# Kernel optimization log

Measured on AMD Instinct MI355X. Metric: run time of the kernel, lower is better.

Reference implementation:

```python
import jax, jax.numpy as jnp
import numpy as np


def gcn_conv(x, src, dst, ew, W, b):
    """PyG GCNConv with edge weights: add self-loops, symmetric deg norm,
    x @ W then normalized scatter-add aggregation, plus bias."""
    N = x.shape[0]
    loop = jnp.arange(N)
    src2 = jnp.concatenate([src, loop])
    dst2 = jnp.concatenate([dst, loop])
    ew2 = jnp.concatenate([ew, jnp.ones((N,), dtype=x.dtype)])
    deg = jax.ops.segment_sum(ew2, dst2, num_segments=N)
    dis = jnp.where(deg > 0, jax.lax.rsqrt(jnp.maximum(deg, 1e-30)), 0.0)
    norm = dis[src2] * ew2 * dis[dst2]            # [E+N]
    h = x @ W                                      # [N, F]
    msg = h[src2] * norm[:, None]                  # gather + scale
    out = jax.ops.segment_sum(msg, dst2, num_segments=N)  # scatter-add
    return out + b


def setup_inputs() -> dict:
    key = jax.random.key(0)
    ks = jax.random.split(key, 12)
    N, F, E, H = 50000, 128, 625000, 121
    x = jax.random.normal(ks[0], (N, F), dtype=jnp.float32)
    edge_index = jax.random.randint(ks[1], (2, E), 0, N, dtype=jnp.int64)
    edge_attr = jax.random.uniform(ks[2], (E,), dtype=jnp.float32)
    s = 1.0 / np.sqrt(F)
    W1 = jax.random.uniform(ks[3], (F, F), minval=-s, maxval=s)
    b1 = jnp.zeros((F,), dtype=jnp.float32)
    W2 = jax.random.uniform(ks[4], (F, F), minval=-s, maxval=s)
    b2 = jnp.zeros((F,), dtype=jnp.float32)
    lw1 = jax.random.uniform(ks[5], (F, H), minval=-s, maxval=s)
    lb1 = jax.random.uniform(ks[6], (H,), minval=-s, maxval=s)
    sh = 1.0 / np.sqrt(H)
    lw2 = jax.random.uniform(ks[7], (H, 1), minval=-sh, maxval=sh)
    lb2 = jax.random.uniform(ks[8], (1,), minval=-sh, maxval=sh)
    return {"x": x, "edge_index": edge_index, "edge_attr": edge_attr,
            "W1": W1, "b1": b1, "W2": W2, "b2": b2,
            "lw1": lw1, "lb1": lb1, "lw2": lw2, "lb2": lb2}


def reference(x, edge_index, edge_attr, W1, b1, W2, b2, lw1, lb1, lw2, lb2):
    src, dst = edge_index[0], edge_index[1]
    h = jax.nn.relu(gcn_conv(x, src, dst, edge_attr, W1, b1))
    h = jax.nn.relu(gcn_conv(h, src, dst, edge_attr, W2, b2))
    g = jnp.mean(h, axis=0)                        # graph readout [F]
    g = jax.nn.relu(g @ lw1 + lb1)
    return g @ lw2 + lb2                           # [1]
```

## Files before the change

kernel.cpp:

```cpp
#include <hip/hip_runtime.h>
#include <hip/hip_bf16.h>

#define FDIM 128
#define ELLW 64
#define CHUNK 4096
#define BKTSH 8
#define CAP 4096

typedef unsigned int uint;
typedef unsigned short ushort;
typedef unsigned char uchar;
typedef __attribute__((ext_vector_type(8))) short bf16x8;
typedef __attribute__((ext_vector_type(4))) float f32x4;

__device__ __forceinline__ ushort f2bf(float f) {
    uint u = __float_as_uint(f);
    return (ushort)((u + 0x7fffu + ((u >> 16) & 1u)) >> 16);
}
__device__ __forceinline__ float bfhi(uint v) { return __uint_as_float(v & 0xffff0000u); }
__device__ __forceinline__ uchar f2fp8(float f) {
    return (uchar)(__builtin_amdgcn_cvt_pk_fp8_f32(f, 0.f, 0, false) & 0xff);
}

__global__ void prep(const float* __restrict__ W1, const float* __restrict__ W2,
                     ushort* __restrict__ wt1, ushort* __restrict__ wt2,
                     int* __restrict__ gcursor, float* __restrict__ partial2,
                     int nbkt) {
    int i = blockIdx.x * 256 + threadIdx.x;
    if (i < 16384) {
        int k = i >> 7, c = i & 127;
        wt1[c * FDIM + k] = f2bf(W1[i]);
    } else {
        int j = i - 16384;
        int k = j >> 7, c = j & 127;
        wt2[c * FDIM + k] = f2bf(W2[j]);
    }
    if (i < nbkt) gcursor[i] = i * CAP;
    if (i < 64 * FDIM) partial2[i] = 0.f;
}

__global__ __launch_bounds__(256)
void build_p1(const int* __restrict__ srcs, const int* __restrict__ dsts,
              const float* __restrict__ ew, int* gcursor,
              uint2* __restrict__ part, int E, int nbkt) {
    __shared__ int hist[256];
    __shared__ int gbase[256];
    __shared__ int cur[256];
    int tid = threadIdx.x;
    hist[tid] = 0;
    __syncthreads();
    int base = blockIdx.x * CHUNK;
    #pragma unroll
    for (int i = 0; i < CHUNK / 256; ++i) {
        int e = base + i * 256 + tid;
        if (e < E) atomicAdd(&hist[dsts[e] >> BKTSH], 1);
    }
    __syncthreads();
    if (tid < nbkt && hist[tid] > 0)
        gbase[tid] = atomicAdd(&gcursor[tid], hist[tid]);
    cur[tid] = 0;
    __syncthreads();
    #pragma unroll
    for (int i = 0; i < CHUNK / 256; ++i) {
        int e = base + i * 256 + tid;
        if (e < E) {
            int d = dsts[e];
            int bkt = d >> BKTSH;
            int pos = atomicAdd(&cur[bkt], 1);
            long gp = (long)gbase[bkt] + pos;
            if (gp < (long)(bkt + 1) * CAP)
                part[gp] = make_uint2(((uint)f2bf(ew[e]) << 16) | (uint)srcs[e],
                                      (uint)d);
        }
    }
}

__global__ __launch_bounds__(256)
void build_p2(const uint2* __restrict__ part, const int* __restrict__ gcursor,
              uint* __restrict__ ell, int* __restrict__ cnt,
              float* __restrict__ dis, int N) {
    __shared__ int lcur[256];
    __shared__ float ldeg[256];
    int tid = threadIdx.x;
    int b = blockIdx.x;
    lcur[tid] = 0; ldeg[tid] = 0.f;
    __syncthreads();
    int start = b * CAP;
    int end = min(gcursor[b], start + CAP);
    for (int e = start + tid; e < end; e += 256) {
        uint2 pe = part[e];
        int li = (int)pe.y - (b << BKTSH);
        int r = atomicAdd(&lcur[li], 1);
        if (r < ELLW) ell[(long)pe.y * ELLW + r] = pe.x;
        atomicAdd(&ldeg[li], bfhi(pe.x));
    }
    __syncthreads();
    int d = (b << BKTSH) + tid;
    if (d < N) {
        cnt[d] = min(lcur[tid], ELLW);
        dis[d] = rsqrtf(1.0f + ldeg[tid]);
    }
}

template<int IN_BF16>
__global__ __launch_bounds__(256) void gemm_mfma(const void* __restrict__ Ap,
                                                 const ushort* __restrict__ Wt,
                                                 const float* __restrict__ dis,
                                                 uchar* __restrict__ Hb, int N) {
    int lane = threadIdx.x & 63;
    int wave = threadIdx.x >> 6;
    int row0 = blockIdx.x * 64 + wave * 16;
    int m = lane & 15;
    int ko = (lane >> 4) << 3;
    int row = row0 + m;

    f32x4 acc[8];
    #pragma unroll
    for (int n = 0; n < 8; ++n) acc[n] = (f32x4){0.f, 0.f, 0.f, 0.f};

    #pragma unroll 1
    for (int kc = 0; kc < FDIM; kc += 32) {
        bf16x8 a = (bf16x8)(short)0;
        if (row < N) {
            if (IN_BF16) {
                a = *(const bf16x8*)((const ushort*)Ap + (long)row * FDIM + kc + ko);
            } else {
                const float* A = (const float*)Ap;
                float4 f0 = *(const float4*)(A + (long)row * FDIM + kc + ko);
                float4 f1 = *(const float4*)(A + (long)row * FDIM + kc + ko + 4);
                a[0] = (short)f2bf(f0.x); a[1] = (short)f2bf(f0.y);
                a[2] = (short)f2bf(f0.z); a[3] = (short)f2bf(f0.w);
                a[4] = (short)f2bf(f1.x); a[5] = (short)f2bf(f1.y);
                a[6] = (short)f2bf(f1.z); a[7] = (short)f2bf(f1.w);
            }
        }
        #pragma unroll
        for (int n = 0; n < 8; ++n) {
            bf16x8 b = *(const bf16x8*)(Wt + (n * 16 + m) * FDIM + kc + ko);
            acc[n] = __builtin_amdgcn_mfma_f32_16x16x32_bf16(a, b, acc[n], 0, 0, 0);
        }
    }

    int rbase = (lane >> 4) << 2;
    #pragma unroll
    for (int r = 0; r < 4; ++r) {
        int gr = row0 + rbase + r;
        if (gr < N) {
            float sc = dis[gr];
            #pragma unroll
            for (int n = 0; n < 8; ++n)
                Hb[(long)gr * FDIM + n * 16 + m] = f2fp8(acc[n][r] * sc);
        }
    }
}

__device__ __forceinline__ void cvt4_acc(uint4 u, float wv,
                                         float4& a0, float4& a1,
                                         float4& a2, float4& a3) {
    auto lo0 = __builtin_amdgcn_cvt_pk_f32_fp8(u.x, false);
    auto hi0 = __builtin_amdgcn_cvt_pk_f32_fp8(u.x, true);
    auto lo1 = __builtin_amdgcn_cvt_pk_f32_fp8(u.y, false);
    auto hi1 = __builtin_amdgcn_cvt_pk_f32_fp8(u.y, true);
    auto lo2 = __builtin_amdgcn_cvt_pk_f32_fp8(u.z, false);
    auto hi2 = __builtin_amdgcn_cvt_pk_f32_fp8(u.z, true);
    auto lo3 = __builtin_amdgcn_cvt_pk_f32_fp8(u.w, false);
    auto hi3 = __builtin_amdgcn_cvt_pk_f32_fp8(u.w, true);
    a0.x = fmaf(lo0[0], wv, a0.x); a0.y = fmaf(lo0[1], wv, a0.y);
    a0.z = fmaf(hi0[0], wv, a0.z); a0.w = fmaf(hi0[1], wv, a0.w);
    a1.x = fmaf(lo1[0], wv, a1.x); a1.y = fmaf(lo1[1], wv, a1.y);
    a1.z = fmaf(hi1[0], wv, a1.z); a1.w = fmaf(hi1[1], wv, a1.w);
    a2.x = fmaf(lo2[0], wv, a2.x); a2.y = fmaf(lo2[1], wv, a2.y);
    a2.z = fmaf(hi2[0], wv, a2.z); a2.w = fmaf(hi2[1], wv, a2.w);
    a3.x = fmaf(lo3[0], wv, a3.x); a3.y = fmaf(lo3[1], wv, a3.y);
    a3.z = fmaf(hi3[0], wv, a3.z); a3.w = fmaf(hi3[1], wv, a3.w);
}

template<int FUSE>
__global__ __launch_bounds__(256)
void aggregate(const uchar* __restrict__ hb,
               const float* __restrict__ dis,
               const float* __restrict__ b,
               const int* __restrict__ cnt,
               const uint* __restrict__ ell,
               ushort* __restrict__ Ob,
               float* __restrict__ partial2, int N) {
    int tid = threadIdx.x;
    int lane = tid & 7;
    int grp = tid >> 3;
    int d = blockIdx.x * 32 + grp;
    int c0 = lane * 16;
    float4 o0, o1, o2, o3;

    if (d < N) {
        float dd = dis[d];
        float4 bv0 = ((const float4*)b)[lane * 4];
        float4 bv1 = ((const float4*)b)[lane * 4 + 1];
        float4 bv2 = ((const float4*)b)[lane * 4 + 2];
        float4 bv3 = ((const float4*)b)[lane * 4 + 3];
        const uint4* row4 = (const uint4*)(ell + (long)d * ELLW);
        int end = cnt[d];
        float4 a0 = make_float4(0.f, 0.f, 0.f, 0.f);
        float4 a1 = a0, a2 = a0, a3 = a0;
        int k = 0;
        if (end > 0) {
            uint4 ev = row4[0];
            for (; k + 3 < end; k += 4) {
                uint4 evn = row4[(k >> 2) + 1];
                int s0 = ev.x & 0xffff, s1 = ev.y & 0xffff;
                int s2 = ev.z & 0xffff, s3 = ev.w & 0xffff;
                float w0 = bfhi(ev.x), w1 = bfhi(ev.y);
                float w2 = bfhi(ev.z), w3 = bfhi(ev.w);
                uint4 u0 = *(const uint4*)(hb + (long)s0 * FDIM + c0);
                uint4 u1 = *(const uint4*)(hb + (long)s1 * FDIM + c0);
                uint4 u2 = *(const uint4*)(hb + (long)s2 * FDIM + c0);
                uint4 u3 = *(const uint4*)(hb + (long)s3 * FDIM + c0);
                cvt4_acc(u0, w0, a0, a1, a2, a3);
                cvt4_acc(u1, w1, a0, a1, a2, a3);
                cvt4_acc(u2, w2, a0, a1, a2, a3);
                cvt4_acc(u3, w3, a0, a1, a2, a3);
                ev = evn;
            }
            for (; k < end; ++k) {
                int q = k & 3;
                uint e0 = (q == 0) ? ev.x : (q == 1) ? ev.y : (q == 2) ? ev.z : ev.w;
                int s0 = e0 & 0xffff;
                float w0 = bfhi(e0);
                uint4 u0 = *(const uint4*)(hb + (long)s0 * FDIM + c0);
                cvt4_acc(u0, w0, a0, a1, a2, a3);
            }
        }
        uint4 ud = *(const uint4*)(hb + (long)d * FDIM + c0);
        cvt4_acc(ud, 1.0f, a0, a1, a2, a3);
        o0.x = fmaxf(fmaf(a0.x, dd, bv0.x), 0.f);
        o0.y = fmaxf(fmaf(a0.y, dd, bv0.y), 0.f);
        o0.z = fmaxf(fmaf(a0.z, dd, bv0.z), 0.f);
        o0.w = fmaxf(fmaf(a0.w, dd, bv0.w), 0.f);
        o1.x = fmaxf(fmaf(a1.x, dd, bv1.x), 0.f);
        o1.y = fmaxf(fmaf(a1.y, dd, bv1.y), 0.f);
        o1.z = fmaxf(fmaf(a1.z, dd, bv1.z), 0.f);
        o1.w = fmaxf(fmaf(a1.w, dd, bv1.w), 0.f);
        o2.x = fmaxf(fmaf(a2.x, dd, bv2.x), 0.f);
        o2.y = fmaxf(fmaf(a2.y, dd, bv2.y), 0.f);
        o2.z = fmaxf(fmaf(a2.z, dd, bv2.z), 0.f);
        o2.w = fmaxf(fmaf(a2.w, dd, bv2.w), 0.f);
        o3.x = fmaxf(fmaf(a3.x, dd, bv3.x), 0.f);
        o3.y = fmaxf(fmaf(a3.y, dd, bv3.y), 0.f);
        o3.z = fmaxf(fmaf(a3.z, dd, bv3.z), 0.f);
        o3.w = fmaxf(fmaf(a3.w, dd, bv3.w), 0.f);
        if (!FUSE) {
            uint4 ov;
            ov.x = (uint)f2bf(o0.x) | ((uint)f2bf(o0.y) << 16);
            ov.y = (uint)f2bf(o0.z) | ((uint)f2bf(o0.w) << 16);
            ov.z = (uint)f2bf(o1.x) | ((uint)f2bf(o1.y) << 16);
            ov.w = (uint)f2bf(o1.z) | ((uint)f2bf(o1.w) << 16);
            *(uint4*)(Ob + (long)d * FDIM + c0) = ov;
            ov.x = (uint)f2bf(o2.x) | ((uint)f2bf(o2.y) << 16);
            ov.y = (uint)f2bf(o2.z) | ((uint)f2bf(o2.w) << 16);
            ov.z = (uint)f2bf(o3.x) | ((uint)f2bf(o3.y) << 16);
            ov.w = (uint)f2bf(o3.z) | ((uint)f2bf(o3.w) << 16);
            *(uint4*)(Ob + (long)d * FDIM + c0 + 8) = ov;
        }
    } else {
        o0 = make_float4(0.f, 0.f, 0.f, 0.f);
        o1 = o0; o2 = o0; o3 = o0;
    }

    if constexpr (FUSE) {
        __shared__ float red[32][FDIM];
        *(float4*)&red[grp][c0]      = o0;
        *(float4*)&red[grp][c0 + 4]  = o1;
        *(float4*)&red[grp][c0 + 8]  = o2;
        *(float4*)&red[grp][c0 + 12] = o3;
        __syncthreads();
        if (tid < FDIM) {
            float s = 0.f;
            #pragma unroll
            for (int gi = 0; gi < 32; ++gi) s += red[gi][tid];
            atomicAdd(&partial2[(blockIdx.x & 63) * FDIM + tid], s);
        }
    }
}

__global__ void mlp_head(const float* __restrict__ partial2,
                         const float* __restrict__ lw1,
                         const float* __restrict__ lb1,
                         const float* __restrict__ lw2,
                         const float* __restrict__ lb2,
                         float* __restrict__ out, float invN, int H) {
    __shared__ float gs[FDIM];
    __shared__ float red[FDIM];
    int t = threadIdx.x;
    float s = 0.f;
    #pragma unroll 8
    for (int r = 0; r < 64; ++r) s += partial2[r * FDIM + t];
    gs[t] = s * invN;
    __syncthreads();
    float p = 0.f;
    if (t < H) {
        float acc = lb1[t];
        #pragma unroll 8
        for (int f = 0; f < FDIM; ++f)
            acc = fmaf(gs[f], lw1[f * H + t], acc);
        p = fmaxf(acc, 0.f) * lw2[t];
    }
    red[t] = p;
    __syncthreads();
    for (int st = 64; st > 0; st >>= 1) {
        if (t < st) red[t] += red[t + st];
        __syncthreads();
    }
    if (t == 0) out[0] = red[0] + lb2[0];
}

extern "C" void kernel_launch(void* const* d_in, const int* in_sizes, int n_in,
                              void* d_out, int out_size, void* d_ws, size_t ws_size,
                              hipStream_t stream) {
    const float* x   = (const float*)d_in[0];
    const int*   eix = (const int*)d_in[1];
    const float* ea  = (const float*)d_in[2];
    const float* W1  = (const float*)d_in[3];
    const float* b1  = (const float*)d_in[4];
    const float* W2  = (const float*)d_in[5];
    const float* b2  = (const float*)d_in[6];
    const float* lw1 = (const float*)d_in[7];
    const float* lb1 = (const float*)d_in[8];
    const float* lw2 = (const float*)d_in[9];
    const float* lb2 = (const float*)d_in[10];

    const int N = in_sizes[0] / FDIM;
    const int E = in_sizes[2];
    const int H = in_sizes[8];
    const int* srcs = eix;
    const int* dsts = eix + E;

    int nAgg = (N + 31) / 32;
    int nbkt = (N + 255) >> 8;

    uchar*  hb      = (uchar*)d_ws;
    ushort* ob      = (ushort*)(hb + (long)N * FDIM);
    ushort* wt1     = ob + (long)N * FDIM;
    ushort* wt2     = wt1 + FDIM * FDIM;
    float*  partial2= (float*)(wt2 + FDIM * FDIM);
    float*  dis     = partial2 + 64 * FDIM;
    uint*   ell     = (uint*)(dis + N);
    int*    cnt     = (int*)(ell + (long)N * ELLW);
    int*    gcursor = cnt + N;
    uint2*  part    = (uint2*)(gcursor + ((nbkt + 1) & ~1));

    float* outv = (float*)d_out;

    int gemmBlocks = (N + 63) / 64;
    int p1Blocks = (E + CHUNK - 1) / CHUNK;

    prep<<<128, 256, 0, stream>>>(W1, W2, wt1, wt2, gcursor, partial2, nbkt);
    build_p1<<<p1Blocks, 256, 0, stream>>>(srcs, dsts, ea, gcursor, part, E, nbkt);
    build_p2<<<nbkt, 256, 0, stream>>>(part, gcursor, ell, cnt, dis, N);

    gemm_mfma<0><<<gemmBlocks, 256, 0, stream>>>(x, wt1, dis, hb, N);
    aggregate<0><<<nAgg, 256, 0, stream>>>(hb, dis, b1, cnt, ell, ob, partial2, N);

    gemm_mfma<1><<<gemmBlocks, 256, 0, stream>>>(ob, wt2, dis, hb, N);
    aggregate<1><<<nAgg, 256, 0, stream>>>(hb, dis, b2, cnt, ell, ob, partial2, N);

    mlp_head<<<1, FDIM, 0, stream>>>(partial2, lw1, lb1, lw2, lb2, outv,
                                     1.0f / (float)N, H);
}
```

Measured before the change: 129.8 us.

## Split fp8 feature matrix into two column halves for cache-friendlier gathers

Result: no change. 131.3 us (+1.1%).

```diff
diff --git a/kernel.cpp b/kernel.cpp
--- a/kernel.cpp
+++ b/kernel.cpp
@@ -148,8 +148,11 @@
         if (gr < N) {
             float sc = dis[gr];
             #pragma unroll
-            for (int n = 0; n < 8; ++n)
-                Hb[(long)gr * FDIM + n * 16 + m] = f2fp8(acc[n][r] * sc);
+            for (int n = 0; n < 8; ++n) {
+                int col = n * 16 + m;
+                Hb[(long)(col >> 6) * N * 64 + (long)gr * 64 + (col & 63)] =
+                    f2fp8(acc[n][r] * sc);
+            }
         }
     }
 }
@@ -185,18 +188,23 @@
                ushort* __restrict__ Ob,
                float* __restrict__ partial2, int N) {
     int tid = threadIdx.x;
-    int lane = tid & 7;
-    int grp = tid >> 3;
-    int d = blockIdx.x * 32 + grp;
+    int lane = tid & 3;
+    int grp = tid >> 2;
+    int bid = blockIdx.x;
+    int half = (bid & 7) >> 2;
+    int tile = (bid >> 3) * 4 + (bid & 3);
+    int d = tile * 64 + grp;
     int c0 = lane * 16;
+    const uchar* hbh = hb + (long)half * N * 64;
     float4 o0, o1, o2, o3;
 
     if (d < N) {
         float dd = dis[d];
-        float4 bv0 = ((const float4*)b)[lane * 4];
-        float4 bv1 = ((const float4*)b)[lane * 4 + 1];
-        float4 bv2 = ((const float4*)b)[lane * 4 + 2];
-        float4 bv3 = ((const float4*)b)[lane * 4 + 3];
+        int cb = (half * 64 + c0) >> 2;
+        float4 bv0 = ((const float4*)b)[cb];
+        float4 bv1 = ((const float4*)b)[cb + 1];
+        float4 bv2 = ((const float4*)b)[cb + 2];
+        float4 bv3 = ((const float4*)b)[cb + 3];
         const uint4* row4 = (const uint4*)(ell + (long)d * ELLW);
         int end = cnt[d];
         float4 a0 = make_float4(0.f, 0.f, 0.f, 0.f);
@@ -210,10 +218,10 @@
                 int s2 = ev.z & 0xffff, s3 = ev.w & 0xffff;
                 float w0 = bfhi(ev.x), w1 = bfhi(ev.y);
                 float w2 = bfhi(ev.z), w3 = bfhi(ev.w);
-                uint4 u0 = *(const uint4*)(hb + (long)s0 * FDIM + c0);
-                uint4 u1 = *(const uint4*)(hb + (long)s1 * FDIM + c0);
-                uint4 u2 = *(const uint4*)(hb + (long)s2 * FDIM + c0);
-                uint4 u3 = *(const uint4*)(hb + (long)s3 * FDIM + c0);
+                uint4 u0 = *(const uint4*)(hbh + (long)s0 * 64 + c0);
+                uint4 u1 = *(const uint4*)(hbh + (long)s1 * 64 + c0);
+                uint4 u2 = *(const uint4*)(hbh + (long)s2 * 64 + c0);
+                uint4 u3 = *(const uint4*)(hbh + (long)s3 * 64 + c0);
                 cvt4_acc(u0, w0, a0, a1, a2, a3);
                 cvt4_acc(u1, w1, a0, a1, a2, a3);
                 cvt4_acc(u2, w2, a0, a1, a2, a3);
@@ -225,11 +233,11 @@
                 uint e0 = (q == 0) ? ev.x : (q == 1) ? ev.y : (q == 2) ? ev.z : ev.w;
                 int s0 = e0 & 0xffff;
                 float w0 = bfhi(e0);
-                uint4 u0 = *(const uint4*)(hb + (long)s0 * FDIM + c0);
+                uint4 u0 = *(const uint4*)(hbh + (long)s0 * 64 + c0);
                 cvt4_acc(u0, w0, a0, a1, a2, a3);
             }
         }
-        uint4 ud = *(const uint4*)(hb + (long)d * FDIM + c0);
+        uint4 ud = *(const uint4*)(hbh + (long)d * 64 + c0);
         cvt4_acc(ud, 1.0f, a0, a1, a2, a3);
         o0.x = fmaxf(fmaf(a0.x, dd, bv0.x), 0.f);
         o0.y = fmaxf(fmaf(a0.y, dd, bv0.y), 0.f);
@@ -248,17 +256,18 @@
         o3.z = fmaxf(fmaf(a3.z, dd, bv3.z), 0.f);
         o3.w = fmaxf(fmaf(a3.w, dd, bv3.w), 0.f);
         if (!FUSE) {
+            int oc = half * 64 + c0;
             uint4 ov;
             ov.x = (uint)f2bf(o0.x) | ((uint)f2bf(o0.y) << 16);
             ov.y = (uint)f2bf(o0.z) | ((uint)f2bf(o0.w) << 16);
             ov.z = (uint)f2bf(o1.x) | ((uint)f2bf(o1.y) << 16);
             ov.w = (uint)f2bf(o1.z) | ((uint)f2bf(o1.w) << 16);
-            *(uint4*)(Ob + (long)d * FDIM + c0) = ov;
+            *(uint4*)(Ob + (long)d * FDIM + oc) = ov;
             ov.x = (uint)f2bf(o2.x) | ((uint)f2bf(o2.y) << 16);
             ov.y = (uint)f2bf(o2.z) | ((uint)f2bf(o2.w) << 16);
             ov.z = (uint)f2bf(o3.x) | ((uint)f2bf(o3.y) << 16);
             ov.w = (uint)f2bf(o3.z) | ((uint)f2bf(o3.w) << 16);
-            *(uint4*)(Ob + (long)d * FDIM + c0 + 8) = ov;
+            *(uint4*)(Ob + (long)d * FDIM + oc + 8) = ov;
         }
     } else {
         o0 = make_float4(0.f, 0.f, 0.f, 0.f);
@@ -266,17 +275,17 @@
     }
 
     if constexpr (FUSE) {
-        __shared__ float red[32][FDIM];
+        __shared__ float red[64][64];
         *(float4*)&red[grp][c0]      = o0;
         *(float4*)&red[grp][c0 + 4]  = o1;
         *(float4*)&red[grp][c0 + 8]  = o2;
         *(float4*)&red[grp][c0 + 12] = o3;
         __syncthreads();
-        if (tid < FDIM) {
+        if (tid < 64) {
             float s = 0.f;
             #pragma unroll
-            for (int gi = 0; gi < 32; ++gi) s += red[gi][tid];
-            atomicAdd(&partial2[(blockIdx.x & 63) * FDIM + tid], s);
+            for (int gi = 0; gi < 64; ++gi) s += red[gi][tid];
+            atomicAdd(&partial2[(bid & 63) * FDIM + half * 64 + tid], s);
         }
     }
 }
@@ -333,7 +342,8 @@
     const int* srcs = eix;
     const int* dsts = eix + E;
 
-    int nAgg = (N + 31) / 32;
+    int nTiles = (N + 63) / 64;
+    int nAgg = ((nTiles + 3) / 4) * 8;
     int nbkt = (N + 255) >> 8;
 
     uchar*  hb      = (uchar*)d_ws;
```
